# Kernel optimization log

Hardware: AMD Instinct MI355X
Metric: run time of the kernel (lower is better)

The kernel has to match this reference:

```python
import jax, jax.numpy as jnp
from jax import lax
import numpy as np

B = 8192
HID = 128
FILT = 256  # stft filter length
HOP = 128
PAD = 64
NBINS = 129  # FILT//2 + 1


def setup_inputs() -> dict:
    key = jax.random.key(0)
    ks = jax.random.split(key, 16)
    def rn(k, shape, fan_in):
        return jax.random.normal(k, shape, dtype=jnp.float32) / np.sqrt(fan_in)
    inp = {
        "audio_input": jax.random.normal(ks[0], (B, 4160), dtype=jnp.float32),
        "hidden_state": jnp.zeros((B, HID), dtype=jnp.float32),
        "cell_state": jnp.zeros((B, HID), dtype=jnp.float32),
        # STFT forward basis: [2*NBINS, 1, FILT] (real then imag banks)
        "stft_w": rn(ks[1], (2 * NBINS, 1, FILT), FILT),
        # encoder: 4 conv1d layers (out, in, k), strides 1,2,2,1, pad 1
        "enc_w1": rn(ks[2], (128, 129, 3), 129 * 3), "enc_b1": jnp.zeros((128,), jnp.float32),
        "enc_w2": rn(ks[3], (64, 128, 3), 128 * 3), "enc_b2": jnp.zeros((64,), jnp.float32),
        "enc_w3": rn(ks[4], (64, 64, 3), 64 * 3),   "enc_b3": jnp.zeros((64,), jnp.float32),
        "enc_w4": rn(ks[5], (128, 64, 3), 64 * 3),  "enc_b4": jnp.zeros((128,), jnp.float32),
        # LSTMCell (PyTorch layout): gates order i,f,g,o
        "w_ih": rn(ks[6], (4 * HID, HID), HID), "w_hh": rn(ks[7], (4 * HID, HID), HID),
        "b_ih": jnp.zeros((4 * HID,), jnp.float32), "b_hh": jnp.zeros((4 * HID,), jnp.float32),
        # output head: Linear(128 -> 1) + sigmoid
        "out_w": rn(ks[8], (1, HID), HID), "out_b": jnp.zeros((1,), jnp.float32),
    }
    return inp


def _conv1d(x, w, b, stride, pad):
    # x: [N, C_in, L], w: [C_out, C_in, k]
    y = lax.conv_general_dilated(x, w, (stride,), [(pad, pad)],
                                 dimension_numbers=("NCH", "OIH", "NCH"))
    return y + b[None, :, None]


def reference(audio_input, hidden_state, cell_state, stft_w,
              enc_w1, enc_b1, enc_w2, enc_b2, enc_w3, enc_b3, enc_w4, enc_b4,
              w_ih, w_hh, b_ih, b_hh, out_w, out_b):
    b = audio_input.shape[0]
    # chunk i with context == audio_input[:, i*512 : i*512 + 576]
    chunks = jnp.stack([audio_input[:, i * 512:i * 512 + 576] for i in range(8)], axis=0)  # [8,B,576]
    x = chunks.reshape(8 * b, 576)
    # STFT: reflect pad 64 each side, conv stride 128 -> [8B, 258, 4]
    xp = jnp.pad(x, ((0, 0), (PAD, PAD)), mode="reflect")[:, None, :]
    spec = lax.conv_general_dilated(xp, stft_w, (HOP,), "VALID",
                                    dimension_numbers=("NCH", "OIH", "NCH"))
    mag = jnp.sqrt(spec[:, :NBINS] ** 2 + spec[:, NBINS:] ** 2)  # [8B,129,4]
    # encoder conv stack: 4 -> 4 -> 2 -> 1 -> 1 frames
    h1 = jax.nn.relu(_conv1d(mag, enc_w1, enc_b1, 1, 1))
    h2 = jax.nn.relu(_conv1d(h1, enc_w2, enc_b2, 2, 1))
    h3 = jax.nn.relu(_conv1d(h2, enc_w3, enc_b3, 2, 1))
    h4 = jax.nn.relu(_conv1d(h3, enc_w4, enc_b4, 1, 1))  # [8B,128,1]
    feats = h4[:, :, 0].reshape(8, b, HID)  # [8,B,128]

    def step(carry, x_t):
        h, c = carry
        gates = x_t @ w_ih.T + b_ih + h @ w_hh.T + b_hh  # [B,4H]
        i_g, f_g, g_g, o_g = jnp.split(gates, 4, axis=-1)
        c_new = jax.nn.sigmoid(f_g) * c + jax.nn.sigmoid(i_g) * jnp.tanh(g_g)
        h_new = jax.nn.sigmoid(o_g) * jnp.tanh(c_new)
        p = jax.nn.sigmoid(h_new @ out_w.T + out_b)  # [B,1]
        return (h_new, c_new), p

    (h_fin, c_fin), probs = lax.scan(step, (hidden_state, cell_state), feats)  # probs [8,B,1]
    # final = 1 - prod_i (1 - p_i), shape [B,1,1]
    final = (1.0 - jnp.prod(1.0 - probs, axis=0))[:, :, None]
    return final, h_fin, c_fin
```

## Files before the change

### kernel.cpp

```cpp
#include <hip/hip_runtime.h>
#include <hip/hip_bf16.h>
#include <math.h>

typedef __hip_bfloat16 bf16;
typedef __attribute__((ext_vector_type(4))) float f32x4;
typedef __attribute__((ext_vector_type(8))) short short8;
typedef __attribute__((ext_vector_type(4))) short short4v;

#define BATCH   8192
#define NTOT    65536
#define NW      262144
#define HID     128

__device__ __forceinline__ float b2f(bf16 v){ return __bfloat162float(v); }
__device__ __forceinline__ bf16  f2b(float v){ return __float2bfloat16(v); }
__device__ __forceinline__ short f2bs(float v){
  bf16 b = __float2bfloat16(v);
  return *reinterpret_cast<short*>(&b);
}
__device__ __forceinline__ float sigf(float x){ return 1.0f/(1.0f+__expf(-x)); }
__device__ __forceinline__ float tanhfast(float x){
  return 1.0f - 2.0f/(__expf(2.0f*x)+1.0f);
}

__global__ __launch_bounds__(256) void k_wcvt(
    const float* __restrict__ W, bf16* __restrict__ Wb)
{
  const int idx = blockIdx.x*256 + threadIdx.x;
  if (idx < 258*256) Wb[idx] = f2b(W[idx]);
}
__global__ __launch_bounds__(256) void k_w1cvt(
    const float* __restrict__ w1, bf16* __restrict__ w1b)
{
  const int idx = blockIdx.x*256 + threadIdx.x;
  if (idx >= 61440) return;
  const int dt = idx / 20480, rem = idx % 20480;
  const int cout = rem / 160, k = rem % 160;
  const float v = (k < 129) ? w1[(cout*129 + k)*3 + dt] : 0.f;
  w1b[idx] = f2b(v);
}
__global__ __launch_bounds__(256) void k_w2cvt(
    const float* __restrict__ w2, bf16* __restrict__ w2b)
{
  const int idx = blockIdx.x*256 + threadIdx.x;
  if (idx >= 24576) return;
  const int dt = idx >> 13, cout = (idx >> 7) & 63, k = idx & 127;
  w2b[idx] = f2b(w2[(cout*128 + k)*3 + dt]);
}
__global__ __launch_bounds__(256) void k_w34cvt(
    const float* __restrict__ w3, const float* __restrict__ w4,
    bf16* __restrict__ w3e, bf16* __restrict__ w4e)
{
  const int idx = blockIdx.x*256 + threadIdx.x;
  if (idx >= 16384) return;
  if (idx < 8192){
    const int row = idx >> 7, k = idx & 127;
    const int cin = k >> 1, t = k & 1;
    w3e[idx] = f2b(w3[(row*64 + cin)*3 + 1 + t]);
  } else {
    const int i2 = idx - 8192;
    const int row = i2 >> 6, cin = i2 & 63;
    w4e[i2] = f2b(w4[(row*64 + cin)*3 + 1]);
  }
}
__global__ __launch_bounds__(256) void k_wlcvt1(
    const float* __restrict__ whh, bf16* __restrict__ wl1)
{
  const int idx = blockIdx.x*256 + threadIdx.x;
  if (idx >= 65536) return;
  wl1[idx] = f2b(whh[idx]);
}
__global__ __launch_bounds__(256) void k_wlxcvt(
    const float* __restrict__ wih, bf16* __restrict__ wlx)
{
  const int idx = blockIdx.x*256 + threadIdx.x;
  if (idx >= 65536) return;
  wlx[idx] = f2b(wih[idx]);
}

__global__ __launch_bounds__(256) void k_stft3(
    const float* __restrict__ audio, const bf16* __restrict__ Wb,
    bf16* __restrict__ mag)
{
  __shared__ __align__(16) char ALDS[96*512];
  __shared__ __align__(16) bf16 refl[4*8*64];
  const int tid = threadIdx.x, lane = tid & 63, wq = tid >> 6;
  const int r0 = blockIdx.x * 4;
  const float* arow = audio + (size_t)(r0 + wq) * 4160;

  #pragma unroll
  for (int q = 0; q < 8; ++q){
    const int e = q*64 + lane;
    const int i = e >> 6, k = e & 63;
    refl[(wq*8 + i)*64 + k] = f2b(arow[512*i + 64 - k]);
  }

  const int kgo8 = (lane>>4)*8;
  short8 Bfrag[2][8];
  #pragma unroll
  for (int ng = 0; ng < 2; ++ng){
    const int wl = ng*16 + (lane & 15);
    const int i = wl >> 2, t = wl & 3;
    #pragma unroll
    for (int ks = 0; ks < 8; ++ks){
      const int kb = ks*32 + kgo8;
      if (t == 0 && kb < 64){
        Bfrag[ng][ks] = *(const short8*)(refl + (wq*8 + i)*64 + kb);
      } else {
        const float* src = arow + 512*i + 128*t - 64 + kb;
        const float4 v0 = *(const float4*)(src);
        const float4 v1 = *(const float4*)(src + 4);
        short8 s;
        s[0]=f2bs(v0.x); s[1]=f2bs(v0.y); s[2]=f2bs(v0.z); s[3]=f2bs(v0.w);
        s[4]=f2bs(v1.x); s[5]=f2bs(v1.y); s[6]=f2bs(v1.z); s[7]=f2bs(v1.w);
        Bfrag[ng][ks] = s;
      }
    }
  }

  const int kab = (lane>>4)*16;
  for (int pass = 0; pass < 3; ++pass){
    __syncthreads();
    for (int idx = tid; idx < 96*32; idx += 256){
      const int ar = idx >> 5;
      const int cb = (idx & 31) * 16;
      const int b3 = ar >> 5, reim = (ar >> 4) & 1, bl = ar & 15;
      int bin = pass*48 + b3*16 + bl;
      if (bin > 128) bin = 128;
      const int grow = bin + reim*129;
      int off = ar*512 + cb; off ^= ((ar&7)<<4);
      *(f32x4*)(ALDS + off) = *(const f32x4*)((const char*)Wb + grow*512 + cb);
    }
    __syncthreads();

    f32x4 accRe[3][2], accIm[3][2];
    #pragma unroll
    for (int b3 = 0; b3 < 3; ++b3)
      #pragma unroll
      for (int ng = 0; ng < 2; ++ng){
        accRe[b3][ng] = f32x4{0.f,0.f,0.f,0.f};
        accIm[b3][ng] = f32x4{0.f,0.f,0.f,0.f};
      }
    #pragma unroll
    for (int ks = 0; ks < 8; ++ks){
      #pragma unroll
      for (int b3 = 0; b3 < 3; ++b3){
        const int arRe = b3*32 + (lane & 15);
        const int arIm = arRe + 16;
        int offRe = arRe*512 + ks*64 + kab; offRe ^= ((arRe&7)<<4);
        int offIm = arIm*512 + ks*64 + kab; offIm ^= ((arIm&7)<<4);
        const short8 aRe = *(const short8*)(ALDS + offRe);
        const short8 aIm = *(const short8*)(ALDS + offIm);
        #pragma unroll
        for (int ng = 0; ng < 2; ++ng){
          accRe[b3][ng] = __builtin_amdgcn_mfma_f32_16x16x32_bf16(
              aRe, Bfrag[ng][ks], accRe[b3][ng], 0, 0, 0);
          accIm[b3][ng] = __builtin_amdgcn_mfma_f32_16x16x32_bf16(
              aIm, Bfrag[ng][ks], accIm[b3][ng], 0, 0, 0);
        }
      }
    }
    #pragma unroll
    for (int b3 = 0; b3 < 3; ++b3)
      #pragma unroll
      for (int j = 0; j < 4; ++j){
        const int bin = (pass*3 + b3)*16 + (lane>>4)*4 + j;
        if (bin <= 128){
          #pragma unroll
          for (int ng = 0; ng < 2; ++ng){
            const int wl = ng*16 + (lane & 15);
            const int i = wl >> 2, t = wl & 3;
            const float re = accRe[b3][ng][j], im = accIm[b3][ng][j];
            mag[(size_t)bin*NW + (size_t)i*32768 + (r0+wq)*4 + t] =
                f2b(sqrtf(re*re + im*im));
          }
        }
      }
  }
}

#define E1_LDS (192*320)
__global__ __launch_bounds__(256) void k_enc1234(
    const bf16* __restrict__ mag,
    const bf16* __restrict__ w1b, const float* __restrict__ b1,
    const bf16* __restrict__ w2b, const float* __restrict__ b2,
    const bf16* __restrict__ w3e, const float* __restrict__ b3,
    const bf16* __restrict__ w4e, const float* __restrict__ b4,
    bf16* __restrict__ h4)
{
  __shared__ __align__(16) char Bs[E1_LDS];
  char* const B3 = Bs + 40960;
  char* const B4 = Bs + 49152;
  const int tid = threadIdx.x, lane = tid & 63, wq = tid >> 6;
  const int n0 = blockIdx.x * 32;
  const int i  = n0 >> 13, b0 = n0 & 8191;
  const size_t colbase = (size_t)i*32768 + (size_t)b0*4;
  const int kb = (lane>>4)*16;
  const int wr = wq >> 1, wc = wq & 1;

  for (int off = tid*16; off < E1_LDS; off += 256*16)
    *(f32x4*)(Bs + off) = f32x4{0.f,0.f,0.f,0.f};
  __syncthreads();
  for (int it = tid; it < 129*64; it += 256){
    const int cin = it >> 6, seg = it & 63;
    const unsigned int pair =
        *(const unsigned int*)(mag + (size_t)cin*NW + colbase + seg*2);
    #pragma unroll
    for (int q = 0; q < 2; ++q){
      const int w = seg*2 + q;
      const int row = (w>>2)*6 + (w&3) + 1;
      int off = row*320 + cin*2; off ^= ((row&7)<<4);
      *(short*)(Bs + off) = (short)((q==0) ? (pair & 0xffff) : (pair >> 16));
    }
  }
  __syncthreads();

  f32x4 acc1[4][4];
  #pragma unroll
  for (int mg = 0; mg < 4; ++mg)
    #pragma unroll
    for (int ng = 0; ng < 4; ++ng) acc1[mg][ng] = f32x4{0.f,0.f,0.f,0.f};
  int brow[4], acol[4];
  #pragma unroll
  for (int ng = 0; ng < 4; ++ng){
    const int w = wc*64 + ng*16 + (lane & 15);
    brow[ng] = (w>>2)*6 + (w&3);
  }
  #pragma unroll
  for (int mg = 0; mg < 4; ++mg) acol[mg] = wr*64 + mg*16 + (lane & 15);

  for (int dt = 0; dt < 3; ++dt){
    #pragma unroll
    for (int ks = 0; ks < 5; ++ks){
      short8 afr[4], bfr[4];
      #pragma unroll
      for (int mg = 0; mg < 4; ++mg)
        afr[mg] = *(const short8*)((const char*)w1b +
            ((dt*128 + acol[mg])*160 + ks*32)*2 + kb);
      #pragma unroll
      for (int ng = 0; ng < 4; ++ng){
        const int row = brow[ng] + dt;
        int off = row*320 + ks*64 + kb; off ^= ((row&7)<<4);
        bfr[ng] = *(const short8*)(Bs + off);
      }
      #pragma unroll
      for (int mg = 0; mg < 4; ++mg)
        #pragma unroll
        for (int ng = 0; ng < 4; ++ng)
          acc1[mg][ng] = __builtin_amdgcn_mfma_f32_16x16x32_bf16(
              afr[mg], bfr[ng], acc1[mg][ng], 0, 0, 0);
    }
  }
  __syncthreads();

  for (int it = tid; it < 32*16; it += 256){
    const int nloc = it >> 4, cb = (it & 15)*16;
    *(f32x4*)(Bs + (nloc*5)*256 + cb) = f32x4{0.f,0.f,0.f,0.f};
  }
  #pragma unroll
  for (int mg = 0; mg < 4; ++mg)
    #pragma unroll
    for (int j = 0; j < 4; ++j){
      const int cout = wr*64 + mg*16 + (lane>>4)*4 + j;
      const float bv = b1[cout];
      #pragma unroll
      for (int ng = 0; ng < 4; ++ng){
        const int w = wc*64 + ng*16 + (lane & 15);
        float v = acc1[mg][ng][j] + bv; v = v > 0.f ? v : 0.f;
        const int row5 = (w>>2)*5 + (w&3) + 1;
        int off = row5*256 + cout*2; off ^= ((row5&7)<<4);
        *(short*)(Bs + off) = f2bs(v);
      }
    }
  __syncthreads();

  f32x4 acc2[2][2];
  #pragma unroll
  for (int mg = 0; mg < 2; ++mg)
    #pragma unroll
    for (int ng = 0; ng < 2; ++ng) acc2[mg][ng] = f32x4{0.f,0.f,0.f,0.f};
  int brow2[2], acol2[2];
  #pragma unroll
  for (int ng = 0; ng < 2; ++ng){
    const int wl = wc*32 + ng*16 + (lane & 15);
    brow2[ng] = (wl>>1)*5 + (wl&1)*2;
  }
  #pragma unroll
  for (int mg = 0; mg < 2; ++mg) acol2[mg] = wr*32 + mg*16 + (lane & 15);

  for (int dt = 0; dt < 3; ++dt){
    #pragma unroll
    for (int ks = 0; ks < 4; ++ks){
      short8 afr[2], bfr[2];
      #pragma unroll
      for (int mg = 0; mg < 2; ++mg)
        afr[mg] = *(const short8*)((const char*)w2b +
            ((dt*64 + acol2[mg])*128 + ks*32)*2 + kb);
      #pragma unroll
      for (int ng = 0; ng < 2; ++ng){
        const int row = brow2[ng] + dt;
        int off = row*256 + ks*64 + kb; off ^= ((row&7)<<4);
        bfr[ng] = *(const short8*)(Bs + off);
      }
      #pragma unroll
      for (int mg = 0; mg < 2; ++mg)
        #pragma unroll
        for (int ng = 0; ng < 2; ++ng)
          acc2[mg][ng] = __builtin_amdgcn_mfma_f32_16x16x32_bf16(
              afr[mg], bfr[ng], acc2[mg][ng], 0, 0, 0);
    }
  }

  #pragma unroll
  for (int mg = 0; mg < 2; ++mg)
    #pragma unroll
    for (int j = 0; j < 4; ++j){
      const int cout2 = wr*32 + mg*16 + (lane>>4)*4 + j;
      const float bv = b2[cout2];
      #pragma unroll
      for (int ng = 0; ng < 2; ++ng){
        const int wl = wc*32 + ng*16 + (lane & 15);
        float v = acc2[mg][ng][j] + bv; v = v > 0.f ? v : 0.f;
        const int nloc = wl >> 1, tp = wl & 1;
        int off = nloc*256 + (cout2*2 + tp)*2; off ^= ((nloc&7)<<4);
        *(short*)(B3 + off) = f2bs(v);
      }
    }
  __syncthreads();

  f32x4 acc3[2];
  acc3[0] = f32x4{0.f,0.f,0.f,0.f};
  acc3[1] = f32x4{0.f,0.f,0.f,0.f};
  const int ar1 = wq*16 + (lane & 15);
  #pragma unroll
  for (int ks = 0; ks < 4; ++ks){
    const short8 a = *(const short8*)((const char*)w3e + (ar1*128 + ks*32)*2 + kb);
    #pragma unroll
    for (int ng = 0; ng < 2; ++ng){
      const int row = ng*16 + (lane & 15);
      int off = row*256 + ks*64 + kb; off ^= ((row&7)<<4);
      const short8 bfr = *(const short8*)(B3 + off);
      acc3[ng] = __builtin_amdgcn_mfma_f32_16x16x32_bf16(a, bfr, acc3[ng], 0, 0, 0);
    }
  }

  #pragma unroll
  for (int j = 0; j < 4; ++j){
    const int r1 = wq*16 + (lane>>4)*4 + j;
    const float bv = b3[r1];
    #pragma unroll
    for (int ng = 0; ng < 2; ++ng){
      const int col = ng*16 + (lane & 15);
      float v = acc3[ng][j] + bv; v = v > 0.f ? v : 0.f;
      int off = col*128 + r1*2; off ^= ((col&7)<<4);
      *(short*)(B4 + off) = f2bs(v);
    }
  }
  __syncthreads();

  f32x4 acc4[2][2];
  #pragma unroll
  for (int mg = 0; mg < 2; ++mg)
    #pragma unroll
    for (int ng = 0; ng < 2; ++ng) acc4[mg][ng] = f32x4{0.f,0.f,0.f,0.f};
  #pragma unroll
  for (int ks = 0; ks < 2; ++ks){
    short8 bfr[2];
    #pragma unroll
    for (int ng = 0; ng < 2; ++ng){
      const int row = ng*16 + (lane & 15);
      int off = row*128 + ks*64 + kb; off ^= ((row&7)<<4);
      bfr[ng] = *(const short8*)(B4 + off);
    }
    #pragma unroll
    for (int mg = 0; mg < 2; ++mg){
      const int ar2 = wq*32 + mg*16 + (lane & 15);
      const short8 a = *(const short8*)((const char*)w4e + (ar2*64 + ks*32)*2 + kb);
      #pragma unroll
      for (int ng = 0; ng < 2; ++ng)
        acc4[mg][ng] = __builtin_amdgcn_mfma_f32_16x16x32_bf16(a, bfr[ng], acc4[mg][ng], 0, 0, 0);
    }
  }
  #pragma unroll
  for (int mg = 0; mg < 2; ++mg)
    #pragma unroll
    for (int j = 0; j < 4; ++j){
      const int cout = wq*32 + mg*16 + (lane>>4)*4 + j;
      const float bv = b4[cout];
      #pragma unroll
      for (int ng = 0; ng < 2; ++ng){
        const int n = n0 + ng*16 + (lane & 15);
        float v = acc4[mg][ng][j] + bv; v = v > 0.f ? v : 0.f;
        h4[(size_t)cout*NTOT + n] = f2b(v);
      }
    }
}

__global__ __launch_bounds__(256) void k_gatex(
    const bf16* __restrict__ h4, const bf16* __restrict__ wlx,
    float* __restrict__ xg, int half)
{
  __shared__ __align__(16) char Bs[32*256];
  const int tid = threadIdx.x, lane = tid & 63, wq = tid >> 6;
  const int n0 = blockIdx.x * 32;
  const int gcol = half*32768 + n0;

  for (int it = tid; it < 128*32; it += 256){
    const int cp = it >> 5, nl = it & 31;
    const bf16 v = h4[(size_t)cp*NTOT + gcol + nl];
    int off = nl*256 + cp*2; off ^= ((nl&7)<<4);
    *(short*)(Bs + off) = *(const short*)&v;
  }
  __syncthreads();

  f32x4 acc[8][2];
  #pragma unroll
  for (int mg = 0; mg < 8; ++mg)
    #pragma unroll
    for (int ng = 0; ng < 2; ++ng) acc[mg][ng] = f32x4{0.f,0.f,0.f,0.f};

  int arow[8];
  #pragma unroll
  for (int mg = 0; mg < 8; ++mg) arow[mg] = wq*128 + mg*16 + (lane & 15);
  const int kb = (lane>>4)*16;

  #pragma unroll
  for (int ks = 0; ks < 4; ++ks){
    short8 bfr[2];
    #pragma unroll
    for (int ng = 0; ng < 2; ++ng){
      const int row = ng*16 + (lane & 15);
      int off = row*256 + ks*64 + kb; off ^= ((row&7)<<4);
      bfr[ng] = *(const short8*)(Bs + off);
    }
    #pragma unroll
    for (int mg = 0; mg < 8; ++mg){
      const short8 a = *(const short8*)((const char*)wlx +
          ((size_t)arow[mg]*128 + ks*32)*2 + kb);
      #pragma unroll
      for (int ng = 0; ng < 2; ++ng)
        acc[mg][ng] = __builtin_amdgcn_mfma_f32_16x16x32_bf16(
            a, bfr[ng], acc[mg][ng], 0, 0, 0);
    }
  }

  #pragma unroll
  for (int mg = 0; mg < 8; ++mg)
    #pragma unroll
    for (int j = 0; j < 4; ++j){
      const int row = wq*128 + mg*16 + (lane>>4)*4 + j;
      #pragma unroll
      for (int ng = 0; ng < 2; ++ng){
        const int col = gcol + ng*16 + (lane & 15);
        xg[(size_t)row*65536 + col] = acc[mg][ng][j];
      }
    }
}

__global__ __launch_bounds__(256) void k_lstm_all2(
    const float* __restrict__ xg, const bf16* __restrict__ wl1,
    const float* __restrict__ bih, const float* __restrict__ bhh,
    const float* __restrict__ h0, const float* __restrict__ c0,
    const float* __restrict__ ow, const float* __restrict__ ob,
    float* __restrict__ out)
{
  __shared__ __align__(16) char Bs[32*256];
  __shared__ float Ppart[16*32];
  __shared__ float Pprod[32];
  const int tid = threadIdx.x, lane = tid & 63, wq = tid >> 6;
  const int b0 = blockIdx.x * 32;
  const int c0r = wq*32;

  for (int it = tid; it < 128*32; it += 256){
    const int cp = it >> 5, bl = it & 31;
    const float v = h0[(size_t)(b0 + bl)*128 + cp];
    int off = bl*256 + cp*2; off ^= ((bl&7)<<4);
    *(short*)(Bs + off) = f2bs(v);
  }
  float cst[2][2][4], bsum[4][2][4], owv[2][4];
  #pragma unroll
  for (int h = 0; h < 2; ++h)
    #pragma unroll
    for (int j = 0; j < 4; ++j){
      const int c = c0r + h*16 + (lane>>4)*4 + j;
      owv[h][j] = ow[c];
      #pragma unroll
      for (int g = 0; g < 4; ++g)
        bsum[g][h][j] = bih[g*128 + c] + bhh[g*128 + c];
      #pragma unroll
      for (int ng = 0; ng < 2; ++ng)
        cst[h][ng][j] = c0[(size_t)(b0 + ng*16 + (lane & 15))*128 + c];
    }
  if (tid < 32) Pprod[tid] = 1.f;
  const float obv = ob[0];

  int arow[4][2];
  #pragma unroll
  for (int g = 0; g < 4; ++g)
    #pragma unroll
    for (int h = 0; h < 2; ++h)
      arow[g][h] = (g*128 + c0r + h*16 + (lane&15))*256 + (lane>>4)*16;

  __syncthreads();

  for (int s = 0; s < 8; ++s){
    f32x4 acc[4][2][2];
    #pragma unroll
    for (int g = 0; g < 4; ++g)
      #pragma unroll
      for (int h = 0; h < 2; ++h)
        #pragma unroll
        for (int ng = 0; ng < 2; ++ng) acc[g][h][ng] = f32x4{0.f,0.f,0.f,0.f};
    #pragma unroll
    for (int ks = 0; ks < 4; ++ks){
      short8 bfr[2];
      #pragma unroll
      for (int ng = 0; ng < 2; ++ng){
        const int row = ng*16 + (lane & 15);
        int off = row*256 + ks*64 + (lane>>4)*16; off ^= ((row&7)<<4);
        bfr[ng] = *(const short8*)(Bs + off);
      }
      #pragma unroll
      for (int g = 0; g < 4; ++g)
        #pragma unroll
        for (int h = 0; h < 2; ++h){
          const short8 a = *(const short8*)((const char*)wl1 + arow[g][h] + ks*64);
          #pragma unroll
          for (int ng = 0; ng < 2; ++ng)
            acc[g][h][ng] = __builtin_amdgcn_mfma_f32_16x16x32_bf16(
                a, bfr[ng], acc[g][h][ng], 0, 0, 0);
        }
    }
    __syncthreads();

    float psum0 = 0.f, psum1 = 0.f;
    #pragma unroll
    for (int h = 0; h < 2; ++h)
      #pragma unroll
      for (int ng = 0; ng < 2; ++ng)
        #pragma unroll
        for (int j = 0; j < 4; ++j){
          const int c = c0r + h*16 + (lane>>4)*4 + j;
          const int b = b0 + ng*16 + (lane & 15);
          const size_t xc = (size_t)s*8192 + b;
          const float ig = acc[0][h][ng][j] + xg[(size_t)(0*128+c)*65536 + xc] + bsum[0][h][j];
          const float fg = acc[1][h][ng][j] + xg[(size_t)(1*128+c)*65536 + xc] + bsum[1][h][j];
          const float gg = acc[2][h][ng][j] + xg[(size_t)(2*128+c)*65536 + xc] + bsum[2][h][j];
          const float og = acc[3][h][ng][j] + xg[(size_t)(3*128+c)*65536 + xc] + bsum[3][h][j];
          const float cn = sigf(fg)*cst[h][ng][j] + sigf(ig)*tanhfast(gg);
          const float hn = sigf(og)*tanhfast(cn);
          cst[h][ng][j] = cn;
          const float pw = owv[h][j] * hn;
          if (ng == 0) psum0 += pw; else psum1 += pw;
          const int bl = ng*16 + (lane & 15);
          int off = bl*256 + c*2; off ^= ((bl&7)<<4);
          *(short*)(Bs + off) = f2bs(hn);
          if (s == 7){
            out[8192 + (size_t)b*128 + c]           = hn;
            out[8192 + 1048576 + (size_t)b*128 + c] = cn;
          }
        }
    Ppart[(wq*4 + (lane>>4))*32 + (lane & 15)]      = psum0;
    Ppart[(wq*4 + (lane>>4))*32 + 16 + (lane & 15)] = psum1;
    __syncthreads();
    if (tid < 32){
      float a2 = obv;
      #pragma unroll
      for (int q2 = 0; q2 < 16; ++q2) a2 += Ppart[q2*32 + tid];
      Pprod[tid] *= (1.f - sigf(a2));
    }
  }
  if (tid < 32) out[b0 + tid] = 1.f - Pprod[tid];
}

extern "C" void kernel_launch(void* const* d_in, const int* in_sizes, int n_in,
                              void* d_out, int out_size, void* d_ws, size_t ws_size,
                              hipStream_t stream)
{
  (void)in_sizes; (void)n_in; (void)out_size; (void)ws_size;
  const float* audio = (const float*)d_in[0];
  const float* h0    = (const float*)d_in[1];
  const float* c0    = (const float*)d_in[2];
  const float* stftw = (const float*)d_in[3];
  const float* w1 = (const float*)d_in[4];  const float* b1 = (const float*)d_in[5];
  const float* w2 = (const float*)d_in[6];  const float* b2 = (const float*)d_in[7];
  const float* w3 = (const float*)d_in[8];  const float* b3 = (const float*)d_in[9];
  const float* w4 = (const float*)d_in[10]; const float* b4 = (const float*)d_in[11];
  const float* wih = (const float*)d_in[12]; const float* whh = (const float*)d_in[13];
  const float* bih = (const float*)d_in[14]; const float* bhh = (const float*)d_in[15];
  const float* ow  = (const float*)d_in[16]; const float* ob  = (const float*)d_in[17];
  float* out = (float*)d_out;

  char* ws = (char*)d_ws;
  float* xg   = (float*)(ws + 0);
  bf16*  mag  = (bf16*) (ws + 0);
  bf16*  h4   = (bf16*) (ws + 134217728);
  bf16*  Wbf  = (bf16*) (ws + 134217728);
  bf16*  w1b  = (bf16*) (ws + 150994944);
  bf16*  w2b  = (bf16*) (ws + 151117824);
  bf16*  w3e  = (bf16*) (ws + 151166976);
  bf16*  w4e  = (bf16*) (ws + 151183360);
  bf16*  wl1  = (bf16*) (ws + 151199744);
  bf16*  wlx  = (bf16*) (ws + 151330816);

  k_wcvt  <<<258, 256, 0, stream>>>(stftw, Wbf);
  k_w1cvt <<<240, 256, 0, stream>>>(w1, w1b);
  k_w2cvt <<<96, 256, 0, stream>>>(w2, w2b);
  k_w34cvt<<<64, 256, 0, stream>>>(w3, w4, w3e, w4e);
  k_wlcvt1<<<256, 256, 0, stream>>>(whh, wl1);
  k_wlxcvt<<<256, 256, 0, stream>>>(wih, wlx);
  k_stft3<<<2048, 256, 0, stream>>>(audio, Wbf, mag);
  k_enc1234<<<2048, 256, 0, stream>>>(mag, w1b, b1, w2b, b2, w3e, b3,
                                      w4e, b4, h4);
  k_gatex<<<1024, 256, 0, stream>>>(h4, wlx, xg, 0);
  k_gatex<<<1024, 256, 0, stream>>>(h4, wlx, xg, 1);
  k_lstm_all2<<<256, 256, 0, stream>>>(xg, wl1, bih, bhh, h0, c0, ow, ob, out);
}
```

Baseline: 430.0 us.

## Merge weight-conversion kernels and halve STFT LDS tile via K-split staging

```diff
diff --git a/kernel.cpp b/kernel.cpp
--- a/kernel.cpp
+++ b/kernel.cpp
@@ -23,66 +23,51 @@
   return 1.0f - 2.0f/(__expf(2.0f*x)+1.0f);
 }
 
-__global__ __launch_bounds__(256) void k_wcvt(
-    const float* __restrict__ W, bf16* __restrict__ Wb)
+__global__ __launch_bounds__(256) void k_allcvt(
+    const float* __restrict__ stftw, const float* __restrict__ w1,
+    const float* __restrict__ w2, const float* __restrict__ w3,
+    const float* __restrict__ w4, const float* __restrict__ whh,
+    const float* __restrict__ wih,
+    bf16* __restrict__ Wbf, bf16* __restrict__ w1b, bf16* __restrict__ w2b,
+    bf16* __restrict__ w3e, bf16* __restrict__ w4e, bf16* __restrict__ wl1,
+    bf16* __restrict__ wlx)
 {
-  const int idx = blockIdx.x*256 + threadIdx.x;
-  if (idx < 258*256) Wb[idx] = f2b(W[idx]);
-}
-__global__ __launch_bounds__(256) void k_w1cvt(
-    const float* __restrict__ w1, bf16* __restrict__ w1b)
-{
-  const int idx = blockIdx.x*256 + threadIdx.x;
-  if (idx >= 61440) return;
-  const int dt = idx / 20480, rem = idx % 20480;
-  const int cout = rem / 160, k = rem % 160;
-  const float v = (k < 129) ? w1[(cout*129 + k)*3 + dt] : 0.f;
-  w1b[idx] = f2b(v);
-}
-__global__ __launch_bounds__(256) void k_w2cvt(
-    const float* __restrict__ w2, bf16* __restrict__ w2b)
-{
-  const int idx = blockIdx.x*256 + threadIdx.x;
-  if (idx >= 24576) return;
-  const int dt = idx >> 13, cout = (idx >> 7) & 63, k = idx & 127;
-  w2b[idx] = f2b(w2[(cout*128 + k)*3 + dt]);
-}
-__global__ __launch_bounds__(256) void k_w34cvt(
-    const float* __restrict__ w3, const float* __restrict__ w4,
-    bf16* __restrict__ w3e, bf16* __restrict__ w4e)
-{
-  const int idx = blockIdx.x*256 + threadIdx.x;
-  if (idx >= 16384) return;
+  int idx = blockIdx.x*256 + threadIdx.x;
+  if (idx < 66048){ Wbf[idx] = f2b(stftw[idx]); return; }
+  idx -= 66048;
+  if (idx < 61440){
+    const int dt = idx / 20480, rem = idx % 20480;
+    const int cout = rem / 160, k = rem % 160;
+    const float v = (k < 129) ? w1[(cout*129 + k)*3 + dt] : 0.f;
+    w1b[idx] = f2b(v); return;
+  }
+  idx -= 61440;
+  if (idx < 24576){
+    const int dt = idx >> 13, cout = (idx >> 7) & 63, k = idx & 127;
+    w2b[idx] = f2b(w2[(cout*128 + k)*3 + dt]); return;
+  }
+  idx -= 24576;
   if (idx < 8192){
     const int row = idx >> 7, k = idx & 127;
     const int cin = k >> 1, t = k & 1;
-    w3e[idx] = f2b(w3[(row*64 + cin)*3 + 1 + t]);
-  } else {
-    const int i2 = idx - 8192;
-    const int row = i2 >> 6, cin = i2 & 63;
-    w4e[i2] = f2b(w4[(row*64 + cin)*3 + 1]);
-  }
-}
-__global__ __launch_bounds__(256) void k_wlcvt1(
-    const float* __restrict__ whh, bf16* __restrict__ wl1)
-{
-  const int idx = blockIdx.x*256 + threadIdx.x;
-  if (idx >= 65536) return;
-  wl1[idx] = f2b(whh[idx]);
-}
-__global__ __launch_bounds__(256) void k_wlxcvt(
-    const float* __restrict__ wih, bf16* __restrict__ wlx)
-{
-  const int idx = blockIdx.x*256 + threadIdx.x;
-  if (idx >= 65536) return;
-  wlx[idx] = f2b(wih[idx]);
+    w3e[idx] = f2b(w3[(row*64 + cin)*3 + 1 + t]); return;
+  }
+  idx -= 8192;
+  if (idx < 8192){
+    const int row = idx >> 6, cin = idx & 63;
+    w4e[idx] = f2b(w4[(row*64 + cin)*3 + 1]); return;
+  }
+  idx -= 8192;
+  if (idx < 65536){ wl1[idx] = f2b(whh[idx]); return; }
+  idx -= 65536;
+  if (idx < 65536){ wlx[idx] = f2b(wih[idx]); return; }
 }
 
 __global__ __launch_bounds__(256) void k_stft3(
     const float* __restrict__ audio, const bf16* __restrict__ Wb,
     bf16* __restrict__ mag)
 {
-  __shared__ __align__(16) char ALDS[96*512];
+  __shared__ __align__(16) char ALDS[96*256];
   __shared__ __align__(16) bf16 refl[4*8*64];
   const int tid = threadIdx.x, lane = tid & 63, wq = tid >> 6;
   const int r0 = blockIdx.x * 4;
@@ -120,19 +105,6 @@
 
   const int kab = (lane>>4)*16;
   for (int pass = 0; pass < 3; ++pass){
-    __syncthreads();
-    for (int idx = tid; idx < 96*32; idx += 256){
-      const int ar = idx >> 5;
-      const int cb = (idx & 31) * 16;
-      const int b3 = ar >> 5, reim = (ar >> 4) & 1, bl = ar & 15;
-      int bin = pass*48 + b3*16 + bl;
-      if (bin > 128) bin = 128;
-      const int grow = bin + reim*129;
-      int off = ar*512 + cb; off ^= ((ar&7)<<4);
-      *(f32x4*)(ALDS + off) = *(const f32x4*)((const char*)Wb + grow*512 + cb);
-    }
-    __syncthreads();
-
     f32x4 accRe[3][2], accIm[3][2];
     #pragma unroll
     for (int b3 = 0; b3 < 3; ++b3)
@@ -142,21 +114,38 @@
         accIm[b3][ng] = f32x4{0.f,0.f,0.f,0.f};
       }
     #pragma unroll
-    for (int ks = 0; ks < 8; ++ks){
-      #pragma unroll
-      for (int b3 = 0; b3 < 3; ++b3){
-        const int arRe = b3*32 + (lane & 15);
-        const int arIm = arRe + 16;
-        int offRe = arRe*512 + ks*64 + kab; offRe ^= ((arRe&7)<<4);
-        int offIm = arIm*512 + ks*64 + kab; offIm ^= ((arIm&7)<<4);
-        const short8 aRe = *(const short8*)(ALDS + offRe);
-        const short8 aIm = *(const short8*)(ALDS + offIm);
+    for (int khalf = 0; khalf < 2; ++khalf){
+      __syncthreads();
+      for (int idx = tid; idx < 96*16; idx += 256){
+        const int ar = idx >> 4;
+        const int cb = (idx & 15) * 16;
+        const int b3 = ar >> 5, reim = (ar >> 4) & 1, bl = ar & 15;
+        int bin = pass*48 + b3*16 + bl;
+        if (bin > 128) bin = 128;
+        const int grow = bin + reim*129;
+        int off = ar*256 + cb; off ^= ((ar&7)<<4);
+        *(f32x4*)(ALDS + off) =
+            *(const f32x4*)((const char*)Wb + grow*512 + khalf*256 + cb);
+      }
+      __syncthreads();
+      #pragma unroll
+      for (int ksl = 0; ksl < 4; ++ksl){
+        const int ks = khalf*4 + ksl;
         #pragma unroll
-        for (int ng = 0; ng < 2; ++ng){
-          accRe[b3][ng] = __builtin_amdgcn_mfma_f32_16x16x32_bf16(
-              aRe, Bfrag[ng][ks], accRe[b3][ng], 0, 0, 0);
-          accIm[b3][ng] = __builtin_amdgcn_mfma_f32_16x16x32_bf16(
-              aIm, Bfrag[ng][ks], accIm[b3][ng], 0, 0, 0);
+        for (int b3 = 0; b3 < 3; ++b3){
+          const int arRe = b3*32 + (lane & 15);
+          const int arIm = arRe + 16;
+          int offRe = arRe*256 + ksl*64 + kab; offRe ^= ((arRe&7)<<4);
+          int offIm = arIm*256 + ksl*64 + kab; offIm ^= ((arIm&7)<<4);
+          const short8 aRe = *(const short8*)(ALDS + offRe);
+          const short8 aIm = *(const short8*)(ALDS + offIm);
+          #pragma unroll
+          for (int ng = 0; ng < 2; ++ng){
+            accRe[b3][ng] = __builtin_amdgcn_mfma_f32_16x16x32_bf16(
+                aRe, Bfrag[ng][ks], accRe[b3][ng], 0, 0, 0);
+            accIm[b3][ng] = __builtin_amdgcn_mfma_f32_16x16x32_bf16(
+                aIm, Bfrag[ng][ks], accIm[b3][ng], 0, 0, 0);
+          }
         }
       }
     }
@@ -603,12 +592,8 @@
   bf16*  wl1  = (bf16*) (ws + 151199744);
   bf16*  wlx  = (bf16*) (ws + 151330816);
 
-  k_wcvt  <<<258, 256, 0, stream>>>(stftw, Wbf);
-  k_w1cvt <<<240, 256, 0, stream>>>(w1, w1b);
-  k_w2cvt <<<96, 256, 0, stream>>>(w2, w2b);
-  k_w34cvt<<<64, 256, 0, stream>>>(w3, w4, w3e, w4e);
-  k_wlcvt1<<<256, 256, 0, stream>>>(whh, wl1);
-  k_wlxcvt<<<256, 256, 0, stream>>>(wih, wlx);
+  k_allcvt<<<1170, 256, 0, stream>>>(stftw, w1, w2, w3, w4, whh, wih,
+                                     Wbf, w1b, w2b, w3e, w4e, wl1, wlx);
   k_stft3<<<2048, 256, 0, stream>>>(audio, Wbf, mag);
   k_enc1234<<<2048, 256, 0, stream>>>(mag, w1b, b1, w2b, b2, w3e, b3,
                                       w4e, b4, h4);
```

Result: no change. 428.7 us (-0.3%).
